# Kernel tuning notes

Hardware: AMD Instinct MI355X
Metric: run time of the kernel (lower is better)

The kernel has to match this reference:

```python
import jax, jax.numpy as jnp
import numpy as np

INPUT_SIZE = 256
HIDDEN_SIZE = 256
B, T = 64, 4096


def setup_inputs() -> dict:
    key = jax.random.key(0)
    k_x, k_ih, k_hh, k_b = jax.random.split(key, 4)
    lim = 1.0 / np.sqrt(HIDDEN_SIZE)  # eqx LSTMCell init range
    xs = jax.random.normal(k_x, (B, T, INPUT_SIZE), dtype=jnp.float32)
    W_ih = jax.random.uniform(k_ih, (4 * HIDDEN_SIZE, INPUT_SIZE), minval=-lim, maxval=lim, dtype=jnp.float32)
    W_hh = jax.random.uniform(k_hh, (4 * HIDDEN_SIZE, HIDDEN_SIZE), minval=-lim, maxval=lim, dtype=jnp.float32)
    b = jax.random.uniform(k_b, (4 * HIDDEN_SIZE,), minval=-lim, maxval=lim, dtype=jnp.float32)
    return {"xs": xs, "W_ih": W_ih, "W_hh": W_hh, "b": b}


def reference(xs, W_ih, W_hh, b):
    # xs: [B, T, D]; eqx.nn.LSTMCell math, scanned over time, vectorized over batch.
    Bsz, Tlen, D = xs.shape
    H = W_hh.shape[1]
    # Precompute input contribution for all timesteps in one big GEMM: [T, B, 4H]
    x_gates = jnp.swapaxes(xs @ W_ih.T + b, 0, 1)

    def step(state, xg):
        h, c = state  # each [B, H]
        gates = xg + h @ W_hh.T  # [B, 4H]
        i, f, g, o = jnp.split(gates, 4, axis=-1)
        c = jax.nn.sigmoid(f) * c + jax.nn.sigmoid(i) * jnp.tanh(g)
        h = jax.nn.sigmoid(o) * jnp.tanh(c)
        return (h, c), None

    init = (jnp.zeros((Bsz, H), xs.dtype), jnp.zeros((Bsz, H), xs.dtype))
    (h, c), _ = jax.lax.scan(step, init, x_gates)
    return (h, c)
```

## Files before the change

### kernel.cpp

```cpp
#include <hip/hip_runtime.h>
#include <hip/hip_fp16.h>
#include <stdint.h>


#define LSTM_B 64
#define LSTM_T 4096
#define LSTM_D 256
#define LSTM_H 256

#define WS_HG_OFF (1u << 20)

typedef __attribute__((ext_vector_type(8))) _Float16 half8;
typedef __attribute__((ext_vector_type(4))) float f32x4;

#define AST64(p, v) __hip_atomic_store((p), (v), __ATOMIC_RELAXED, __HIP_MEMORY_SCOPE_AGENT)
#define ALD64(p)    __hip_atomic_load((p), __ATOMIC_RELAXED, __HIP_MEMORY_SCOPE_AGENT)
#define BARLG()     asm volatile("s_waitcnt lgkmcnt(0)\n\ts_barrier" ::: "memory")

static __device__ __forceinline__ float sigmoidf_(float x) {
    return 1.0f / (1.0f + __expf(-x));
}
static __device__ __forceinline__ float tanhf_(float x) {
    float ax = fabsf(x);
    float e  = __expf(-2.0f * ax);
    float t  = (1.0f - e) / (1.0f + e);
    return copysignf(t, x);
}

__global__ __launch_bounds__(256) void prep_frags(
    const float* __restrict__ W_ih, const float* __restrict__ W_hh,
    uint8_t* __restrict__ ws)
{
    int idx = blockIdx.x * blockDim.x + threadIdx.x;
    uint4* Wp = (uint4*)ws;
    int lane = idx & 63;
    int kk   = (idx >> 6) & 15;
    int T    = idx >> 10;
    int n  = T * 16 + (lane & 15);
    int r  = ((n & 3) << 8) + (n >> 2);
    int kb = 32 * kk + 4 * (lane >> 4);
    uint32_t u[4];
    #pragma unroll
    for (int h = 0; h < 4; ++h) {
        uint32_t lohi[2];
        #pragma unroll
        for (int e = 0; e < 2; ++e) {
            int j = 2 * h + e;
            int k = kb + (j & 3) + 16 * (j >> 2);
            float v = (k < 256) ? W_hh[r * 256 + k] : W_ih[r * 256 + (k - 256)];
            lohi[e] = (uint32_t)__half_as_ushort(__float2half(v));
        }
        u[h] = lohi[0] | (lohi[1] << 16);
    }
    Wp[idx] = make_uint4(u[0], u[1], u[2], u[3]);
    if (idx < 32768) ((uint32_t*)(ws + WS_HG_OFF))[idx] = 0u;
}

__global__ __launch_bounds__(256, 1) void lstm_r11(
    const float* __restrict__ xs,
    const float* __restrict__ bias_g,
    uint8_t* __restrict__ ws,
    float* __restrict__ out)
{
    const int tid = threadIdx.x;
    const int l   = tid & 63;
    const int w   = tid >> 6;
    const int g   = blockIdx.x & 7;
    const int p   = blockIdx.x >> 3;

    const uint4* WF = (const uint4*)ws;
    uint64_t* hg64  = (uint64_t*)(ws + WS_HG_OFF);

    __shared__ uint4 hx[16 * 64];

    uint4 wf[4][16];
    #pragma unroll
    for (int tl = 0; tl < 4; ++tl) {
        int T = p * 16 + w * 4 + tl;
        #pragma unroll
        for (int kk = 0; kk < 16; ++kk)
            wf[tl][kk] = WF[(T * 16 + kk) * 64 + l];
    }
    #pragma unroll
    for (int tl = 0; tl < 4; ++tl)
        #pragma unroll
        for (int kk = 0; kk < 16; ++kk)
            asm volatile("" : "+v"(wf[tl][kk].x), "+v"(wf[tl][kk].y),
                              "+v"(wf[tl][kk].z), "+v"(wf[tl][kk].w));

    const int  c2   = l & 3;
    const int  qa   = l >> 4;
    const bool c2b0 = (c2 & 1) != 0, c2b1 = (c2 & 2) != 0;
    const int  m_ew = 4 * qa + c2;
    float bias[4];
    int   jj[4];
    #pragma unroll
    for (int tl = 0; tl < 4; ++tl) {
        int T    = p * 16 + w * 4 + tl;
        int slot = T * 16 + (l & 15);
        int r    = ((slot & 3) << 8) + (slot >> 2);
        bias[tl] = bias_g[r];
        jj[tl]   = slot >> 2;
    }

    const int m_s = tid >> 4;
    const int d0  = (tid & 15) * 16;
    const float* xrow = xs + (size_t)(8 * g + (m_s & 7)) * LSTM_T * LSTM_D + d0;

    hx[tid]       = make_uint4(0, 0, 0, 0);
    hx[tid + 256] = make_uint4(0, 0, 0, 0);
    hx[tid + 512] = make_uint4(0, 0, 0, 0);
    hx[tid + 768] = make_uint4(0, 0, 0, 0);
    float4 xb[2][4];
    if (m_s < 8) {
        #pragma unroll
        for (int i = 0; i < 4; ++i) {
            float4 xv = ((const float4*)xrow)[i];
            __half2 h0 = __floats2half2_rn(xv.x, xv.y);
            __half2 h1 = __floats2half2_rn(xv.z, xv.w);
            uint64_t v = (uint64_t)__builtin_bit_cast(uint32_t, h0)
                       | ((uint64_t)__builtin_bit_cast(uint32_t, h1) << 32);
            int k0 = 256 + d0 + 4 * i;
            int kk = k0 >> 5, off = k0 & 31;
            int q = (off & 15) >> 2, hi = off >> 4;
            int slot = (m_s + 16 * q) ^ ((2 * kk) & 63);
            *(uint64_t*)((uint8_t*)hx + kk * 1024 + slot * 16 + hi * 8) = v;
        }
        #pragma unroll
        for (int i = 0; i < 4; ++i) xb[0][i] = ((const float4*)(xrow + (size_t)1 * LSTM_D))[i];
        #pragma unroll
        for (int i = 0; i < 4; ++i) xb[1][i] = ((const float4*)(xrow + (size_t)2 * LSTM_D))[i];
    }
    BARLG();

    float cst[4] = {0, 0, 0, 0}, hst[4] = {0, 0, 0, 0};

#define STEP(T_, PAR) do {                                                          \
                                        \
    uint4 af[16];                                                                   \
    _Pragma("unroll")                                                               \
    for (int kk = 0; kk < 16; ++kk)                                                 \
        af[kk] = hx[kk * 64 + (l ^ ((2 * kk) & 63))];                               \
    BARLG();                                                                        \
                         \
    if (m_s < 8) {                                                                  \
        _Pragma("unroll")                                                           \
        for (int i = 0; i < 4; ++i) {                                               \
            float4 xv = xb[PAR][i];                                                 \
            __half2 h0 = __floats2half2_rn(xv.x, xv.y);                             \
            __half2 h1 = __floats2half2_rn(xv.z, xv.w);                             \
            uint64_t v = (uint64_t)__builtin_bit_cast(uint32_t, h0)                 \
                       | ((uint64_t)__builtin_bit_cast(uint32_t, h1) << 32);        \
            int k0 = 256 + d0 + 4 * i;                                              \
            int kk = k0 >> 5, off = k0 & 31;                                        \
            int q = (off & 15) >> 2, hi = off >> 4;                                 \
            int slot = (m_s + 16 * q) ^ ((2 * kk) & 63);                            \
            *(uint64_t*)((uint8_t*)hx + kk * 1024 + slot * 16 + hi * 8) = v;        \
        }                                                                           \
        int tn = (T_ + 3 < LSTM_T) ? T_ + 3 : T_;                                   \
        const float4* nx = (const float4*)(xrow + (size_t)tn * LSTM_D);             \
        _Pragma("unroll")                                                           \
        for (int i = 0; i < 4; ++i) xb[PAR][i] = nx[i];                             \
    }                                                                               \
                                                \
    f32x4 acc[4];                                                                   \
    _Pragma("unroll")                                                               \
    for (int tl = 0; tl < 4; ++tl)                                                  \
        acc[tl] = (f32x4){bias[tl], bias[tl], bias[tl], bias[tl]};                  \
    _Pragma("unroll")                                                               \
    for (int kk = 0; kk < 16; ++kk) {                                               \
        half8 a = __builtin_bit_cast(half8, af[kk]);                                \
        _Pragma("unroll")                                                           \
        for (int tl = 0; tl < 4; ++tl)                                              \
            acc[tl] = __builtin_amdgcn_mfma_f32_16x16x32_f16(                       \
                a, __builtin_bit_cast(half8, wf[tl][kk]), acc[tl], 0, 0, 0);        \
    }                                                                               \
                           \
    uint32_t hpair[4];                                                              \
    _Pragma("unroll")                                                               \
    for (int tl = 0; tl < 4; ++tl) {                                                \
        f32x4 a = acc[tl];                                                          \
        float s01  = c2b0 ? a.y : a.x;                                              \
        float s23  = c2b0 ? a.w : a.z;                                              \
        float s01b = c2b0 ? a.x : a.y;                                              \
        float s23b = c2b0 ? a.z : a.w;                                              \
        float own = c2b1 ? s23  : s01;                                              \
        float v1  = c2b1 ? s23b : s01b;                                             \
        float v2  = c2b1 ? s01  : s23;                                              \
        float v3  = c2b1 ? s01b : s23b;                                             \
        float r1 = __shfl_xor(v1, 1, 64);                                           \
        float r2 = __shfl_xor(v2, 2, 64);                                           \
        float r3 = __shfl_xor(v3, 3, 64);                                           \
        float gi = c2b1 ? (c2b0 ? r3 : r2) : (c2b0 ? r1 : own);                     \
        float gf = c2b1 ? (c2b0 ? r2 : r3) : (c2b0 ? own : r1);                     \
        float gg = c2b1 ? (c2b0 ? r1 : own) : (c2b0 ? r3 : r2);                     \
        float go = c2b1 ? (c2b0 ? own : r1) : (c2b0 ? r2 : r3);                     \
        float cc = cst[tl];                                                         \
        cc = sigmoidf_(gf) * cc + sigmoidf_(gi) * tanhf_(gg);                       \
        float hh = sigmoidf_(go) * tanhf_(cc);                                      \
        cst[tl] = cc; hst[tl] = hh;                                                 \
        uint32_t u  = (uint32_t)__half_as_ushort(__float2half(hh));                 \
        uint32_t up = (uint32_t)__shfl_xor((int)u, 4, 64);                          \
        hpair[tl] = (u & 0xffffu) | (up << 16);                                     \
    }                                                                               \
             \
    {                                                                               \
        const int buf = (PAR) ^ 1;                                                  \
        if (l < 32 && (l & 4) == 0) {                                               \
            uint64_t* hgrow = hg64 + (((size_t)g * 2 + buf) * 8 + m_ew) * 128;      \
            const uint64_t tagw = ((uint64_t)(uint32_t)(T_ + 1)) << 32;             \
            _Pragma("unroll")                                                       \
            for (int tl = 0; tl < 4; ++tl)                                          \
                AST64(&hgrow[jj[tl] >> 1], tagw | (uint64_t)hpair[tl]);             \
        }                                                                           \
                 \
        if (m_s < 8) {                                                              \
            const uint32_t tgt = (uint32_t)(T_ + 1);                                \
            uint64_t* hgr = hg64 + (((size_t)g * 2 + buf) * 8 + m_s) * 128          \
                          + (d0 >> 1);                                              \
            uint64_t hv[8];                                                         \
            _Pragma("unroll")                                                       \
            for (int i = 0; i < 8; ++i) hv[i] = ALD64(&hgr[i]);                     \
            int spin = 0;                                                           \
            while (true) {                                                          \
                bool ok = true;                                                     \
                _Pragma("unroll")                                                   \
                for (int i = 0; i < 8; ++i) ok &= ((uint32_t)(hv[i] >> 32) >= tgt); \
                if (ok || ++spin > 2000) break;                                     \
                _Pragma("unroll")                                                   \
                for (int i = 0; i < 8; ++i) hv[i] = ALD64(&hgr[i]);                 \
            }                                                                       \
            _Pragma("unroll")                                                       \
            for (int i = 0; i < 8; ++i) {                                           \
                uint32_t pr = (uint32_t)hv[i];                                      \
                int k0 = d0 + 2 * i;                                                \
                int kk = k0 >> 5, off = k0 & 31;                                    \
                int q = (off & 15) >> 2, hi = off >> 4;                             \
                int slot = (m_s + 16 * q) ^ ((2 * kk) & 63);                        \
                *(uint32_t*)((uint8_t*)hx + kk * 1024 + slot * 16 + hi * 8          \
                             + ((off & 3) << 1)) = pr;                              \
            }                                                                       \
        }                                                                           \
        BARLG();                                                                    \
    }                                                                               \
} while (0)

    for (int t = 0; t < LSTM_T; t += 2) {
        STEP(t, 0);
        STEP(t + 1, 1);
    }
#undef STEP

    if (m_ew < 8) {
        #pragma unroll
        for (int tl = 0; tl < 4; ++tl) {
            int gb = 8 * g + m_ew;
            out[gb * LSTM_H + jj[tl]]                   = hst[tl];
            out[LSTM_B * LSTM_H + gb * LSTM_H + jj[tl]] = cst[tl];
        }
    }
}

extern "C" void kernel_launch(void* const* d_in, const int* in_sizes, int n_in,
                              void* d_out, int out_size, void* d_ws, size_t ws_size,
                              hipStream_t stream) {
    const float* xs   = (const float*)d_in[0];
    const float* W_ih = (const float*)d_in[1];
    const float* W_hh = (const float*)d_in[2];
    const float* b    = (const float*)d_in[3];
    float* out = (float*)d_out;
    uint8_t* ws = (uint8_t*)d_ws;

    prep_frags<<<256, 256, 0, stream>>>(W_ih, W_hh, ws);
    lstm_r11<<<32, 256, 0, stream>>>(xs, b, ws, out);
}
```

Before: 13.05 ms.

## Precompute next-step input-projection MFMAs off the recurrent critical path

Splits the per-step GEMM into its h-dependent half (k<256) and x-dependent half (k>=256). The x half for step t+1 is now computed with double-buffered accumulators during step t, after x is written to shared memory and before or while the cross-block h exchange spin-wait runs. Only the W_hh MFMAs then remain on the serial recurrence path. This adds accumulator registers and moves the x staging and barrier around the global handoff.

```diff
diff --git a/kernel.cpp b/kernel.cpp
--- a/kernel.cpp
+++ b/kernel.cpp
@@ -56,7 +56,7 @@
     if (idx < 32768) ((uint32_t*)(ws + WS_HG_OFF))[idx] = 0u;
 }
 
-__global__ __launch_bounds__(256, 1) void lstm_r11(
+__global__ __launch_bounds__(256, 1) void lstm_r13(
     const float* __restrict__ xs,
     const float* __restrict__ bias_g,
     uint8_t* __restrict__ ws,
@@ -133,53 +133,47 @@
     }
     BARLG();
 
+    f32x4 accA[4], accB[4];
+    {
+        uint4 afx[8];
+        #pragma unroll
+        for (int kx = 0; kx < 8; ++kx) {
+            int kk = kx + 8;
+            afx[kx] = hx[kk * 64 + (l ^ ((2 * kk) & 63))];
+        }
+        #pragma unroll
+        for (int tl = 0; tl < 4; ++tl)
+            accA[tl] = (f32x4){bias[tl], bias[tl], bias[tl], bias[tl]};
+        #pragma unroll
+        for (int kx = 0; kx < 8; ++kx) {
+            half8 a = __builtin_bit_cast(half8, afx[kx]);
+            #pragma unroll
+            for (int tl = 0; tl < 4; ++tl)
+                accA[tl] = __builtin_amdgcn_mfma_f32_16x16x32_f16(
+                    a, __builtin_bit_cast(half8, wf[tl][kx + 8]), accA[tl], 0, 0, 0);
+        }
+    }
+
     float cst[4] = {0, 0, 0, 0}, hst[4] = {0, 0, 0, 0};
 
-#define STEP(T_, PAR) do {                                                          \
-                                        \
-    uint4 af[16];                                                                   \
+#define STEP(T_, PAR, ACC_C, ACC_N) do {                                            \
+                    \
+    uint4 afh[8];                                                                   \
     _Pragma("unroll")                                                               \
-    for (int kk = 0; kk < 16; ++kk)                                                 \
-        af[kk] = hx[kk * 64 + (l ^ ((2 * kk) & 63))];                               \
-    BARLG();                                                                        \
-                         \
-    if (m_s < 8) {                                                                  \
-        _Pragma("unroll")                                                           \
-        for (int i = 0; i < 4; ++i) {                                               \
-            float4 xv = xb[PAR][i];                                                 \
-            __half2 h0 = __floats2half2_rn(xv.x, xv.y);                             \
-            __half2 h1 = __floats2half2_rn(xv.z, xv.w);                             \
-            uint64_t v = (uint64_t)__builtin_bit_cast(uint32_t, h0)                 \
-                       | ((uint64_t)__builtin_bit_cast(uint32_t, h1) << 32);        \
-            int k0 = 256 + d0 + 4 * i;                                              \
-            int kk = k0 >> 5, off = k0 & 31;                                        \
-            int q = (off & 15) >> 2, hi = off >> 4;                                 \
-            int slot = (m_s + 16 * q) ^ ((2 * kk) & 63);                            \
-            *(uint64_t*)((uint8_t*)hx + kk * 1024 + slot * 16 + hi * 8) = v;        \
-        }                                                                           \
-        int tn = (T_ + 3 < LSTM_T) ? T_ + 3 : T_;                                   \
-        const float4* nx = (const float4*)(xrow + (size_t)tn * LSTM_D);             \
-        _Pragma("unroll")                                                           \
-        for (int i = 0; i < 4; ++i) xb[PAR][i] = nx[i];                             \
-    }                                                                               \
-                                                \
-    f32x4 acc[4];                                                                   \
+    for (int kk = 0; kk < 8; ++kk)                                                  \
+        afh[kk] = hx[kk * 64 + (l ^ ((2 * kk) & 63))];                              \
     _Pragma("unroll")                                                               \
-    for (int tl = 0; tl < 4; ++tl)                                                  \
-        acc[tl] = (f32x4){bias[tl], bias[tl], bias[tl], bias[tl]};                  \
-    _Pragma("unroll")                                                               \
-    for (int kk = 0; kk < 16; ++kk) {                                               \
-        half8 a = __builtin_bit_cast(half8, af[kk]);                                \
+    for (int kk = 0; kk < 8; ++kk) {                                                \
+        half8 a = __builtin_bit_cast(half8, afh[kk]);                               \
         _Pragma("unroll")                                                           \
         for (int tl = 0; tl < 4; ++tl)                                              \
-            acc[tl] = __builtin_amdgcn_mfma_f32_16x16x32_f16(                       \
-                a, __builtin_bit_cast(half8, wf[tl][kk]), acc[tl], 0, 0, 0);        \
+            ACC_C[tl] = __builtin_amdgcn_mfma_f32_16x16x32_f16(                     \
+                a, __builtin_bit_cast(half8, wf[tl][kk]), ACC_C[tl], 0, 0, 0);      \
     }                                                                               \
-                           \
     uint32_t hpair[4];                                                              \
     _Pragma("unroll")                                                               \
     for (int tl = 0; tl < 4; ++tl) {                                                \
-        f32x4 a = acc[tl];                                                          \
+        f32x4 a = ACC_C[tl];                                                        \
         float s01  = c2b0 ? a.y : a.x;                                              \
         float s23  = c2b0 ? a.w : a.z;                                              \
         float s01b = c2b0 ? a.x : a.y;                                              \
@@ -203,7 +197,6 @@
         uint32_t up = (uint32_t)__shfl_xor((int)u, 4, 64);                          \
         hpair[tl] = (u & 0xffffu) | (up << 16);                                     \
     }                                                                               \
-             \
     {                                                                               \
         const int buf = (PAR) ^ 1;                                                  \
         if (l < 32 && (l & 4) == 0) {                                               \
@@ -213,7 +206,35 @@
             for (int tl = 0; tl < 4; ++tl)                                          \
                 AST64(&hgrow[jj[tl] >> 1], tagw | (uint64_t)hpair[tl]);             \
         }                                                                           \
-                 \
+                            \
+        if (m_s < 8) {                                                              \
+            _Pragma("unroll")                                                       \
+            for (int i = 0; i < 4; ++i) {                                           \
+                float4 xv = xb[PAR][i];                                             \
+                __half2 h0 = __floats2half2_rn(xv.x, xv.y);                         \
+                __half2 h1 = __floats2half2_rn(xv.z, xv.w);                         \
+                uint64_t v = (uint64_t)__builtin_bit_cast(uint32_t, h0)             \
+                           | ((uint64_t)__builtin_bit_cast(uint32_t, h1) << 32);    \
+                int k0 = 256 + d0 + 4 * i;                                          \
+                int kk = k0 >> 5, off = k0 & 31;                                    \
+                int q = (off & 15) >> 2, hi = off >> 4;                             \
+                int slot = (m_s + 16 * q) ^ ((2 * kk) & 63);                        \
+                *(uint64_t*)((uint8_t*)hx + kk * 1024 + slot * 16 + hi * 8) = v;    \
+            }                                                                       \
+            int tn = (T_ + 3 < LSTM_T) ? T_ + 3 : T_;                               \
+            const float4* nx = (const float4*)(xrow + (size_t)tn * LSTM_D);         \
+            _Pragma("unroll")                                                       \
+            for (int i = 0; i < 4; ++i) xb[PAR][i] = nx[i];                         \
+        }                                                                           \
+        BARLG();          \
+                                      \
+        uint4 afx[8];                                                               \
+        _Pragma("unroll")                                                           \
+        for (int kx = 0; kx < 8; ++kx) {                                            \
+            int kk = kx + 8;                                                        \
+            afx[kx] = hx[kk * 64 + (l ^ ((2 * kk) & 63))];                          \
+        }                                                                           \
+            \
         if (m_s < 8) {                                                              \
             const uint32_t tgt = (uint32_t)(T_ + 1);                                \
             uint64_t* hgr = hg64 + (((size_t)g * 2 + buf) * 8 + m_s) * 128          \
@@ -241,13 +262,26 @@
                              + ((off & 3) << 1)) = pr;                              \
             }                                                                       \
         }                                                                           \
-        BARLG();                                                                    \
+                    \
+        _Pragma("unroll")                                                           \
+        for (int tl = 0; tl < 4; ++tl)                                              \
+            ACC_N[tl] = (f32x4){bias[tl], bias[tl], bias[tl], bias[tl]};            \
+        _Pragma("unroll")                                                           \
+        for (int kx = 0; kx < 8; ++kx) {                                            \
+            half8 a = __builtin_bit_cast(half8, afx[kx]);                           \
+            _Pragma("unroll")                                                       \
+            for (int tl = 0; tl < 4; ++tl)                                          \
+                ACC_N[tl] = __builtin_amdgcn_mfma_f32_16x16x32_f16(                 \
+                    a, __builtin_bit_cast(half8, wf[tl][kx + 8]), ACC_N[tl],        \
+                    0, 0, 0);                                                       \
+        }                                                                           \
+        BARLG();              \
     }                                                                               \
 } while (0)
 
     for (int t = 0; t < LSTM_T; t += 2) {
-        STEP(t, 0);
-        STEP(t + 1, 1);
+        STEP(t,     0, accA, accB);
+        STEP(t + 1, 1, accB, accA);
     }
 #undef STEP
 
@@ -272,5 +306,5 @@
     uint8_t* ws = (uint8_t*)d_ws;
 
     prep_frags<<<256, 256, 0, stream>>>(W_ih, W_hh, ws);
-    lstm_r11<<<32, 256, 0, stream>>>(xs, b, ws, out);
-}
+    lstm_r13<<<32, 256, 0, stream>>>(xs, b, ws, out);
+}
```

After: 12.35 ms. 5.3% less time.

## Interleave two batch groups per block and precompute input-projection half off critical path

Applied to the files above, without the earlier changes.

Each block now handles two batch groups (A and B) with separate LDS buffers and accumulators, halving the grid from 32 to 16 blocks. The steps of the two groups are interleaved so that one group's cross-block spin-wait overlaps the other group's compute. The x-contribution MFMAs (k=256..511) are computed right after the h exchange for the next step, so only the h half of the GEMM sits on the recurrent critical path. The cost is twice the serial work per block, more register pressure from two accumulator sets, and a longer spin-timeout bound.

```diff
diff --git a/kernel.cpp b/kernel.cpp
--- a/kernel.cpp
+++ b/kernel.cpp
@@ -56,7 +56,7 @@
     if (idx < 32768) ((uint32_t*)(ws + WS_HG_OFF))[idx] = 0u;
 }
 
-__global__ __launch_bounds__(256, 1) void lstm_r11(
+__global__ __launch_bounds__(256, 1) void lstm_r14(
     const float* __restrict__ xs,
     const float* __restrict__ bias_g,
     uint8_t* __restrict__ ws,
@@ -65,13 +65,17 @@
     const int tid = threadIdx.x;
     const int l   = tid & 63;
     const int w   = tid >> 6;
-    const int g   = blockIdx.x & 7;
-    const int p   = blockIdx.x >> 3;
+    const int G   = blockIdx.x & 3;
+    const int p   = blockIdx.x >> 2;
+    const int gA  = 2 * G;
+    const int gB  = 2 * G + 1;
 
     const uint4* WF = (const uint4*)ws;
     uint64_t* hg64  = (uint64_t*)(ws + WS_HG_OFF);
 
-    __shared__ uint4 hx[16 * 64];
+    __shared__ uint4 hx2[2 * 16 * 64];
+    uint8_t* hxA = (uint8_t*)hx2;
+    uint8_t* hxB = (uint8_t*)hx2 + 16384;
 
     uint4 wf[4][16];
     #pragma unroll
@@ -105,81 +109,115 @@
 
     const int m_s = tid >> 4;
     const int d0  = (tid & 15) * 16;
-    const float* xrow = xs + (size_t)(8 * g + (m_s & 7)) * LSTM_T * LSTM_D + d0;
-
-    hx[tid]       = make_uint4(0, 0, 0, 0);
-    hx[tid + 256] = make_uint4(0, 0, 0, 0);
-    hx[tid + 512] = make_uint4(0, 0, 0, 0);
-    hx[tid + 768] = make_uint4(0, 0, 0, 0);
-    float4 xb[2][4];
+    const float* xrowA = xs + (size_t)(8 * gA + (m_s & 7)) * LSTM_T * LSTM_D + d0;
+    const float* xrowB = xs + (size_t)(8 * gB + (m_s & 7)) * LSTM_T * LSTM_D + d0;
+
+    #pragma unroll
+    for (int i = 0; i < 8; ++i)
+        hx2[tid + i * 256] = make_uint4(0, 0, 0, 0);
+    float4 xbA[4], xbB[4];
     if (m_s < 8) {
         #pragma unroll
         for (int i = 0; i < 4; ++i) {
-            float4 xv = ((const float4*)xrow)[i];
-            __half2 h0 = __floats2half2_rn(xv.x, xv.y);
-            __half2 h1 = __floats2half2_rn(xv.z, xv.w);
-            uint64_t v = (uint64_t)__builtin_bit_cast(uint32_t, h0)
-                       | ((uint64_t)__builtin_bit_cast(uint32_t, h1) << 32);
+            float4 xvA = ((const float4*)xrowA)[i];
+            float4 xvB = ((const float4*)xrowB)[i];
             int k0 = 256 + d0 + 4 * i;
             int kk = k0 >> 5, off = k0 & 31;
             int q = (off & 15) >> 2, hi = off >> 4;
             int slot = (m_s + 16 * q) ^ ((2 * kk) & 63);
-            *(uint64_t*)((uint8_t*)hx + kk * 1024 + slot * 16 + hi * 8) = v;
-        }
-        #pragma unroll
-        for (int i = 0; i < 4; ++i) xb[0][i] = ((const float4*)(xrow + (size_t)1 * LSTM_D))[i];
-        #pragma unroll
-        for (int i = 0; i < 4; ++i) xb[1][i] = ((const float4*)(xrow + (size_t)2 * LSTM_D))[i];
+            __half2 a0 = __floats2half2_rn(xvA.x, xvA.y);
+            __half2 a1 = __floats2half2_rn(xvA.z, xvA.w);
+            uint64_t va = (uint64_t)__builtin_bit_cast(uint32_t, a0)
+                        | ((uint64_t)__builtin_bit_cast(uint32_t, a1) << 32);
+            *(uint64_t*)(hxA + kk * 1024 + slot * 16 + hi * 8) = va;
+            __half2 b0 = __floats2half2_rn(xvB.x, xvB.y);
+            __half2 b1 = __floats2half2_rn(xvB.z, xvB.w);
+            uint64_t vb = (uint64_t)__builtin_bit_cast(uint32_t, b0)
+                        | ((uint64_t)__builtin_bit_cast(uint32_t, b1) << 32);
+            *(uint64_t*)(hxB + kk * 1024 + slot * 16 + hi * 8) = vb;
+        }
+        #pragma unroll
+        for (int i = 0; i < 4; ++i) {
+            xbA[i] = ((const float4*)(xrowA + (size_t)1 * LSTM_D))[i];
+            xbB[i] = ((const float4*)(xrowB + (size_t)1 * LSTM_D))[i];
+        }
     }
     BARLG();
 
-    float cst[4] = {0, 0, 0, 0}, hst[4] = {0, 0, 0, 0};
-
-#define STEP(T_, PAR) do {                                                          \
-                                        \
-    uint4 af[16];                                                                   \
-    _Pragma("unroll")                                                               \
-    for (int kk = 0; kk < 16; ++kk)                                                 \
-        af[kk] = hx[kk * 64 + (l ^ ((2 * kk) & 63))];                               \
-    BARLG();                                                                        \
-                         \
+    f32x4 accA[4], accB[4];
+    #pragma unroll
+    for (int tl = 0; tl < 4; ++tl) {
+        accA[tl] = (f32x4){bias[tl], bias[tl], bias[tl], bias[tl]};
+        accB[tl] = accA[tl];
+    }
+    #pragma unroll
+    for (int kx = 0; kx < 8; ++kx) {
+        int kk = kx + 8;
+        uint4 fa = *(const uint4*)(hxA + (kk * 64 + (l ^ ((2 * kk) & 63))) * 16);
+        uint4 fb = *(const uint4*)(hxB + (kk * 64 + (l ^ ((2 * kk) & 63))) * 16);
+        #pragma unroll
+        for (int tl = 0; tl < 4; ++tl) {
+            accA[tl] = __builtin_amdgcn_mfma_f32_16x16x32_f16(
+                __builtin_bit_cast(half8, fa), __builtin_bit_cast(half8, wf[tl][kk]), accA[tl], 0, 0, 0);
+            accB[tl] = __builtin_amdgcn_mfma_f32_16x16x32_f16(
+                __builtin_bit_cast(half8, fb), __builtin_bit_cast(half8, wf[tl][kk]), accB[tl], 0, 0, 0);
+        }
+    }
+
+    float cstA[4] = {0, 0, 0, 0}, hstA[4] = {0, 0, 0, 0};
+    float cstB[4] = {0, 0, 0, 0}, hstB[4] = {0, 0, 0, 0};
+
+#define PHASE(GID, HXB, ACC, CST, HST, XB, XROW, T_) do {                           \
+               \
     if (m_s < 8) {                                                                  \
-        _Pragma("unroll")                                                           \
-        for (int i = 0; i < 4; ++i) {                                               \
-            float4 xv = xb[PAR][i];                                                 \
-            __half2 h0 = __floats2half2_rn(xv.x, xv.y);                             \
-            __half2 h1 = __floats2half2_rn(xv.z, xv.w);                             \
-            uint64_t v = (uint64_t)__builtin_bit_cast(uint32_t, h0)                 \
-                       | ((uint64_t)__builtin_bit_cast(uint32_t, h1) << 32);        \
-            int k0 = 256 + d0 + 4 * i;                                              \
+        const int bufp = (T_) & 1;                                                  \
+        const uint32_t tgt = (uint32_t)(T_);                                        \
+        uint64_t* hgr = hg64 + (((size_t)(GID) * 2 + bufp) * 8 + m_s) * 128         \
+                      + (d0 >> 1);                                                  \
+        uint64_t hv[8];                                                             \
+        _Pragma("unroll")                                                           \
+        for (int i = 0; i < 8; ++i) hv[i] = ALD64(&hgr[i]);                         \
+        int spin = 0;                                                               \
+        while (true) {                                                              \
+            bool ok = true;                                                         \
+            _Pragma("unroll")                                                       \
+            for (int i = 0; i < 8; ++i) ok &= ((uint32_t)(hv[i] >> 32) >= tgt);     \
+            if (ok || ++spin > 4000) break;                                         \
+            _Pragma("unroll")                                                       \
+            for (int i = 0; i < 8; ++i) hv[i] = ALD64(&hgr[i]);                     \
+        }                                                                           \
+        _Pragma("unroll")                                                           \
+        for (int i = 0; i < 8; ++i) {                                               \
+            uint32_t pr = (uint32_t)hv[i];                                          \
+            int k0 = d0 + 2 * i;                                                    \
             int kk = k0 >> 5, off = k0 & 31;                                        \
             int q = (off & 15) >> 2, hi = off >> 4;                                 \
             int slot = (m_s + 16 * q) ^ ((2 * kk) & 63);                            \
-            *(uint64_t*)((uint8_t*)hx + kk * 1024 + slot * 16 + hi * 8) = v;        \
-        }                                                                           \
-        int tn = (T_ + 3 < LSTM_T) ? T_ + 3 : T_;                                   \
-        const float4* nx = (const float4*)(xrow + (size_t)tn * LSTM_D);             \
-        _Pragma("unroll")                                                           \
-        for (int i = 0; i < 4; ++i) xb[PAR][i] = nx[i];                             \
-    }                                                                               \
-                                                \
-    f32x4 acc[4];                                                                   \
-    _Pragma("unroll")                                                               \
-    for (int tl = 0; tl < 4; ++tl)                                                  \
-        acc[tl] = (f32x4){bias[tl], bias[tl], bias[tl], bias[tl]};                  \
-    _Pragma("unroll")                                                               \
-    for (int kk = 0; kk < 16; ++kk) {                                               \
-        half8 a = __builtin_bit_cast(half8, af[kk]);                                \
-        _Pragma("unroll")                                                           \
-        for (int tl = 0; tl < 4; ++tl)                                              \
-            acc[tl] = __builtin_amdgcn_mfma_f32_16x16x32_f16(                       \
-                a, __builtin_bit_cast(half8, wf[tl][kk]), acc[tl], 0, 0, 0);        \
-    }                                                                               \
-                           \
+            *(uint32_t*)((HXB) + kk * 1024 + slot * 16 + hi * 8                     \
+                         + ((off & 3) << 1)) = pr;                                  \
+        }                                                                           \
+    }                                                                               \
+    BARLG();                                                                        \
+                                 \
+    {                                                                               \
+        uint4 afh[8];                                                               \
+        _Pragma("unroll")                                                           \
+        for (int kk = 0; kk < 8; ++kk)                                              \
+            afh[kk] = *(const uint4*)((HXB) + (kk * 64 + (l ^ ((2 * kk) & 63))) * 16);\
+        _Pragma("unroll")                                                           \
+        for (int kk = 0; kk < 8; ++kk) {                                            \
+            half8 a = __builtin_bit_cast(half8, afh[kk]);                           \
+            _Pragma("unroll")                                                       \
+            for (int tl = 0; tl < 4; ++tl)                                          \
+                ACC[tl] = __builtin_amdgcn_mfma_f32_16x16x32_f16(                   \
+                    a, __builtin_bit_cast(half8, wf[tl][kk]), ACC[tl], 0, 0, 0);    \
+        }                                                                           \
+    }                                                                               \
+                                           \
     uint32_t hpair[4];                                                              \
     _Pragma("unroll")                                                               \
     for (int tl = 0; tl < 4; ++tl) {                                                \
-        f32x4 a = acc[tl];                                                          \
+        f32x4 a = ACC[tl];                                                          \
         float s01  = c2b0 ? a.y : a.x;                                              \
         float s23  = c2b0 ? a.w : a.z;                                              \
         float s01b = c2b0 ? a.x : a.y;                                              \
@@ -195,68 +233,83 @@
         float gf = c2b1 ? (c2b0 ? r2 : r3) : (c2b0 ? own : r1);                     \
         float gg = c2b1 ? (c2b0 ? r1 : own) : (c2b0 ? r3 : r2);                     \
         float go = c2b1 ? (c2b0 ? own : r1) : (c2b0 ? r2 : r3);                     \
-        float cc = cst[tl];                                                         \
+        float cc = CST[tl];                                                         \
         cc = sigmoidf_(gf) * cc + sigmoidf_(gi) * tanhf_(gg);                       \
         float hh = sigmoidf_(go) * tanhf_(cc);                                      \
-        cst[tl] = cc; hst[tl] = hh;                                                 \
+        CST[tl] = cc; HST[tl] = hh;                                                 \
         uint32_t u  = (uint32_t)__half_as_ushort(__float2half(hh));                 \
         uint32_t up = (uint32_t)__shfl_xor((int)u, 4, 64);                          \
         hpair[tl] = (u & 0xffffu) | (up << 16);                                     \
     }                                                                               \
-             \
+                          \
     {                                                                               \
-        const int buf = (PAR) ^ 1;                                                  \
+        const int bufn = ((T_) + 1) & 1;                                            \
         if (l < 32 && (l & 4) == 0) {                                               \
-            uint64_t* hgrow = hg64 + (((size_t)g * 2 + buf) * 8 + m_ew) * 128;      \
-            const uint64_t tagw = ((uint64_t)(uint32_t)(T_ + 1)) << 32;             \
+            uint64_t* hgrow = hg64 + (((size_t)(GID) * 2 + bufn) * 8 + m_ew) * 128; \
+            const uint64_t tagw = ((uint64_t)(uint32_t)((T_) + 1)) << 32;           \
             _Pragma("unroll")                                                       \
             for (int tl = 0; tl < 4; ++tl)                                          \
                 AST64(&hgrow[jj[tl] >> 1], tagw | (uint64_t)hpair[tl]);             \
         }                                                                           \
-                 \
-        if (m_s < 8) {                                                              \
-            const uint32_t tgt = (uint32_t)(T_ + 1);                                \
-            uint64_t* hgr = hg64 + (((size_t)g * 2 + buf) * 8 + m_s) * 128          \
-                          + (d0 >> 1);                                              \
-            uint64_t hv[8];                                                         \
-            _Pragma("unroll")                                                       \
-            for (int i = 0; i < 8; ++i) hv[i] = ALD64(&hgr[i]);                     \
-            int spin = 0;                                                           \
-            while (true) {                                                          \
-                bool ok = true;                                                     \
-                _Pragma("unroll")                                                   \
-                for (int i = 0; i < 8; ++i) ok &= ((uint32_t)(hv[i] >> 32) >= tgt); \
-                if (ok || ++spin > 2000) break;                                     \
-                _Pragma("unroll")                                                   \
-                for (int i = 0; i < 8; ++i) hv[i] = ALD64(&hgr[i]);                 \
-            }                                                                       \
-            _Pragma("unroll")                                                       \
-            for (int i = 0; i < 8; ++i) {                                           \
-                uint32_t pr = (uint32_t)hv[i];                                      \
-                int k0 = d0 + 2 * i;                                                \
-                int kk = k0 >> 5, off = k0 & 31;                                    \
-                int q = (off & 15) >> 2, hi = off >> 4;                             \
-                int slot = (m_s + 16 * q) ^ ((2 * kk) & 63);                        \
-                *(uint32_t*)((uint8_t*)hx + kk * 1024 + slot * 16 + hi * 8          \
-                             + ((off & 3) << 1)) = pr;                              \
-            }                                                                       \
-        }                                                                           \
-        BARLG();                                                                    \
+    }                                                                               \
+                                        \
+    if (m_s < 8) {                                                                  \
+        _Pragma("unroll")                                                           \
+        for (int i = 0; i < 4; ++i) {                                               \
+            float4 xv = XB[i];                                                      \
+            __half2 h0 = __floats2half2_rn(xv.x, xv.y);                             \
+            __half2 h1 = __floats2half2_rn(xv.z, xv.w);                             \
+            uint64_t v = (uint64_t)__builtin_bit_cast(uint32_t, h0)                 \
+                       | ((uint64_t)__builtin_bit_cast(uint32_t, h1) << 32);        \
+            int k0 = 256 + d0 + 4 * i;                                              \
+            int kk = k0 >> 5, off = k0 & 31;                                        \
+            int q = (off & 15) >> 2, hi = off >> 4;                                 \
+            int slot = (m_s + 16 * q) ^ ((2 * kk) & 63);                            \
+            *(uint64_t*)((HXB) + kk * 1024 + slot * 16 + hi * 8) = v;               \
+        }                                                                           \
+        int tn = ((T_) + 2 < LSTM_T) ? (T_) + 2 : LSTM_T - 1;                       \
+        const float4* nx = (const float4*)((XROW) + (size_t)tn * LSTM_D);           \
+        _Pragma("unroll")                                                           \
+        for (int i = 0; i < 4; ++i) XB[i] = nx[i];                                  \
+    }                                                                               \
+    BARLG();                                                                        \
+                \
+    {                                                                               \
+        uint4 afx[8];                                                               \
+        _Pragma("unroll")                                                           \
+        for (int kx = 0; kx < 8; ++kx) {                                            \
+            int kk = kx + 8;                                                        \
+            afx[kx] = *(const uint4*)((HXB) + (kk * 64 + (l ^ ((2 * kk) & 63))) * 16);\
+        }                                                                           \
+        _Pragma("unroll")                                                           \
+        for (int tl = 0; tl < 4; ++tl)                                              \
+            ACC[tl] = (f32x4){bias[tl], bias[tl], bias[tl], bias[tl]};              \
+        _Pragma("unroll")                                                           \
+        for (int kx = 0; kx < 8; ++kx) {                                            \
+            half8 a = __builtin_bit_cast(half8, afx[kx]);                           \
+            _Pragma("unroll")                                                       \
+            for (int tl = 0; tl < 4; ++tl)                                          \
+                ACC[tl] = __builtin_amdgcn_mfma_f32_16x16x32_f16(                   \
+                    a, __builtin_bit_cast(half8, wf[tl][kx + 8]), ACC[tl], 0, 0, 0);\
+        }                                                                           \
     }                                                                               \
 } while (0)
 
-    for (int t = 0; t < LSTM_T; t += 2) {
-        STEP(t, 0);
-        STEP(t + 1, 1);
-    }
-#undef STEP
+    for (int t = 0; t < LSTM_T; ++t) {
+        PHASE(gA, hxA, accA, cstA, hstA, xbA, xrowA, t);
+        PHASE(gB, hxB, accB, cstB, hstB, xbB, xrowB, t);
+    }
+#undef PHASE
 
     if (m_ew < 8) {
         #pragma unroll
         for (int tl = 0; tl < 4; ++tl) {
-            int gb = 8 * g + m_ew;
-            out[gb * LSTM_H + jj[tl]]                   = hst[tl];
-            out[LSTM_B * LSTM_H + gb * LSTM_H + jj[tl]] = cst[tl];
+            int ba = 8 * gA + m_ew;
+            int bb = 8 * gB + m_ew;
+            out[ba * LSTM_H + jj[tl]]                   = hstA[tl];
+            out[LSTM_B * LSTM_H + ba * LSTM_H + jj[tl]] = cstA[tl];
+            out[bb * LSTM_H + jj[tl]]                   = hstB[tl];
+            out[LSTM_B * LSTM_H + bb * LSTM_H + jj[tl]] = cstB[tl];
         }
     }
 }
@@ -272,5 +325,5 @@
     uint8_t* ws = (uint8_t*)d_ws;
 
     prep_frags<<<256, 256, 0, stream>>>(W_ih, W_hh, ws);
-    lstm_r11<<<32, 256, 0, stream>>>(xs, b, ws, out);
-}
+    lstm_r14<<<16, 256, 0, stream>>>(xs, b, ws, out);
+}
```

Result: slower. 24.79 ms (+90.0%).
